# Performance work log

Measured on AMD Instinct MI355X. Metric: run time of the kernel, lower is better.

The kernel has to match this reference:

```python
import jax, jax.numpy as jnp
import numpy as np

N = 100000   # nodes
E = 1600000  # edges (avg degree 16)
DIM = 3      # coordinate dims
R = 3        # pseudo-coordinate dim
C = 32       # channels / Gaussian kernels
F = 64       # non-coordinate node features


def setup_inputs() -> dict:
    key = jax.random.key(0)
    k1, k2, k3, k4, k5 = jax.random.split(key, 5)
    features = jax.random.normal(k1, (N, DIM + F), dtype=jnp.float32)
    edge_index = jax.random.randint(k2, (E, 2), 0, N, dtype=jnp.int32)  # (row=i, col=j) per edge
    w_dense = jax.random.normal(k3, (DIM, R), dtype=jnp.float32) / jnp.sqrt(jnp.float32(DIM))  # lecun-ish
    b_dense = jnp.zeros((R,), dtype=jnp.float32)
    mu = jax.random.normal(k4, (C, N, R), dtype=jnp.float32) * 0.1
    # sigma initialized positive (abs of lecun normal in the original); keep bounded away from 0
    sig = jax.random.uniform(k5, (C, N, R), dtype=jnp.float32, minval=0.1, maxval=1.0)
    return {"features": features, "edge_index": edge_index,
            "w_dense": w_dense, "b_dense": b_dense, "mu": mu, "sig": sig}


def reference(features, edge_index, w_dense, b_dense, mu, sig):
    coords = features[:, :DIM]          # [N, 3]
    h = features[:, DIM:]               # [N, F]
    src = edge_index[:, 0]              # row index i per edge
    dst = edge_index[:, 1]              # col index j per edge
    # per-edge pseudo-coordinates: tanh(Dense_r(x_j - x_i))
    u = jnp.tanh((coords[dst] - coords[src]) @ w_dense + b_dense)      # [E, R]
    # Gaussian-mixture edge weight per (channel, edge), mu/sigma gathered at row node i
    diff = u[None, :, :] - mu[:, src, :]                               # [C, E, R]
    w = jnp.exp(-0.5 * jnp.sum(diff * diff / sig[:, src, :], axis=-1)) # [C, E]
    # (A o W) @ H summed over feature axis == sum_j w[c,i,j] * sum_f H[j,f]
    msg = w * jnp.sum(h, axis=-1)[dst][None, :]                        # [C, E]
    agg = jax.ops.segment_sum(msg.T, src, num_segments=N)              # [N, C]
    return jnp.concatenate([coords, agg], axis=-1)                     # [N, DIM + C]
```

## Files before the change

kernel.cpp:

```cpp
#include <hip/hip_runtime.h>

#define DIMV 3
#define RV 3
#define CV 32
#define FV 64
#define ROWF 67
#define ROWO 35
#define CAP 64
#define SCAN_T 1024

__device__ __forceinline__ float fast_tanh(float x) {
    float ex = __expf(2.0f * x);
    return (ex - 1.0f) * __builtin_amdgcn_rcpf(ex + 1.0f);
}

__global__ void prep_kernel(const float* __restrict__ features,
                            float4* __restrict__ nd,
                            int* __restrict__ counts,
                            float* __restrict__ out, int N) {
    int gid = blockIdx.x * blockDim.x + threadIdx.x;
    if (gid < N) counts[gid] = 0;
    int node = gid >> 6;
    int lane = threadIdx.x & 63;
    if (node >= N) return;
    const float* row = features + (size_t)node * ROWF;
    float f0 = row[lane];
    float f1 = (lane < ROWF - 64) ? row[64 + lane] : 0.0f;
    float v = (lane >= DIMV ? f0 : 0.0f) + f1;
    for (int off = 32; off > 0; off >>= 1) v += __shfl_xor(v, off, 64);
    float c0 = __shfl(f0, 0, 64);
    float c1 = __shfl(f0, 1, 64);
    float c2 = __shfl(f0, 2, 64);
    if (lane == 0) nd[node] = make_float4(c0, c1, c2, v);
    if (lane < DIMV) out[(size_t)node * ROWO + lane] = f0;
}

__global__ void scatter_pad_kernel(const int2* __restrict__ ei2,
                                   const float4* __restrict__ nd,
                                   const float* __restrict__ wd,
                                   const float* __restrict__ bd,
                                   int* __restrict__ counts,
                                   float4* __restrict__ ue_pad, int E) {
    int e = blockIdx.x * blockDim.x + threadIdx.x;
    if (e >= E) return;
    int2 sd = ei2[e];
    int k = atomicAdd(counts + sd.x, 1);
    if (k >= CAP) k = CAP - 1;
    float4 ps = nd[sd.x];
    float4 pd = nd[sd.y];
    float dx = pd.x - ps.x, dy = pd.y - ps.y, dz = pd.z - ps.z;
    float u0 = fast_tanh(dx * wd[0] + dy * wd[3] + dz * wd[6] + bd[0]);
    float u1 = fast_tanh(dx * wd[1] + dy * wd[4] + dz * wd[7] + bd[1]);
    float u2 = fast_tanh(dx * wd[2] + dy * wd[5] + dz * wd[8] + bd[2]);
    ue_pad[(size_t)sd.x * CAP + k] = make_float4(u0, u1, u2, pd.w);
}

__global__ void node_pad_kernel(const int* __restrict__ counts,
                                const float4* __restrict__ ue_pad,
                                const float* __restrict__ mu,
                                const float* __restrict__ sig,
                                float* __restrict__ out, int N) {
    __shared__ float4 sm[4][CAP];
    int node = (blockIdx.x * blockDim.x + threadIdx.x) >> 6;
    int lane = threadIdx.x & 63;
    int w = threadIdx.x >> 6;
    int c = lane & 31;
    int half = lane >> 5;
    bool valid = node < N;
    float m0 = 0, m1 = 0, m2 = 0, i0 = 1, i1 = 1, i2 = 1;
    int cnt = 0;
    if (valid) {
        size_t slab = (size_t)N * RV;
        const float* mp = mu + (size_t)c * slab + (size_t)node * RV;
        const float* sp = sig + (size_t)c * slab + (size_t)node * RV;
        m0 = mp[0]; m1 = mp[1]; m2 = mp[2];
        i0 = __builtin_amdgcn_rcpf(sp[0]);
        i1 = __builtin_amdgcn_rcpf(sp[1]);
        i2 = __builtin_amdgcn_rcpf(sp[2]);
        cnt = counts[node];
        if (cnt > CAP) cnt = CAP;
        if (lane < cnt) sm[w][lane] = ue_pad[(size_t)node * CAP + lane];
    }
    __syncthreads();
    float acc = 0.0f;
    for (int k = half; k < cnt; k += 2) {
        float4 q = sm[w][k];
        float d0 = q.x - m0, d1 = q.y - m1, d2 = q.z - m2;
        float t = d0 * d0 * i0 + d1 * d1 * i1 + d2 * d2 * i2;
        acc += __expf(-0.5f * t) * q.w;
    }
    acc += __shfl_xor(acc, 32, 64);
    if (valid && half == 0) out[(size_t)node * ROWO + DIMV + c] = acc;
}


__global__ void hist_kernel(const int2* __restrict__ ei2, int* __restrict__ counts, int E) {
    int e = blockIdx.x * blockDim.x + threadIdx.x;
    if (e >= E) return;
    atomicAdd(counts + ei2[e].x, 1);
}

__global__ void scan_a_kernel(const int* __restrict__ counts, int* __restrict__ offsets,
                              int* __restrict__ partials, int N) {
    __shared__ int sm[SCAN_T];
    int t = threadIdx.x;
    int i = blockIdx.x * SCAN_T + t;
    int c = (i < N) ? counts[i] : 0;
    sm[t] = c;
    __syncthreads();
    for (int off = 1; off < SCAN_T; off <<= 1) {
        int v = (t >= off) ? sm[t - off] : 0;
        __syncthreads();
        sm[t] += v;
        __syncthreads();
    }
    if (i < N) offsets[i] = sm[t] - c;
    if (t == SCAN_T - 1) partials[blockIdx.x] = sm[t];
}

__global__ void scan_b_kernel(int* __restrict__ partials, int B) {
    __shared__ int sm[SCAN_T];
    int t = threadIdx.x;
    int c = (t < B) ? partials[t] : 0;
    sm[t] = c;
    __syncthreads();
    for (int off = 1; off < SCAN_T; off <<= 1) {
        int v = (t >= off) ? sm[t - off] : 0;
        __syncthreads();
        sm[t] += v;
        __syncthreads();
    }
    if (t < B) partials[t] = sm[t] - c;
}

__global__ void scan_c_kernel(int* __restrict__ offsets, const int* __restrict__ partials,
                              int* __restrict__ cursor, int N, int E) {
    int i = blockIdx.x * blockDim.x + threadIdx.x;
    if (i == 0) offsets[N] = E;
    if (i >= N) return;
    int off = offsets[i] + partials[i / SCAN_T];
    offsets[i] = off;
    cursor[i] = off;
}

__global__ void scatter_u_kernel(const int2* __restrict__ ei2, int* __restrict__ cursor,
                                 const float4* __restrict__ nd,
                                 const float* __restrict__ wd, const float* __restrict__ bd,
                                 float4* __restrict__ ue, int E) {
    int e = blockIdx.x * blockDim.x + threadIdx.x;
    if (e >= E) return;
    int2 sd = ei2[e];
    int pos = atomicAdd(cursor + sd.x, 1);
    float4 ps = nd[sd.x];
    float4 pd = nd[sd.y];
    float dx = pd.x - ps.x, dy = pd.y - ps.y, dz = pd.z - ps.z;
    float u0 = fast_tanh(dx * wd[0] + dy * wd[3] + dz * wd[6] + bd[0]);
    float u1 = fast_tanh(dx * wd[1] + dy * wd[4] + dz * wd[7] + bd[1]);
    float u2 = fast_tanh(dx * wd[2] + dy * wd[5] + dz * wd[8] + bd[2]);
    ue[pos] = make_float4(u0, u1, u2, pd.w);
}

__global__ void node_acc2_kernel(const int* __restrict__ offsets,
                                 const float4* __restrict__ ue,
                                 const float* __restrict__ mu,
                                 const float* __restrict__ sig,
                                 float* __restrict__ out, int N) {
    int node = (blockIdx.x * blockDim.x + threadIdx.x) >> 6;
    if (node >= N) return;
    int lane = threadIdx.x & 63;
    int c = lane & 31;
    int half = lane >> 5;
    size_t slab = (size_t)N * RV;
    const float* mp = mu + (size_t)c * slab + (size_t)node * RV;
    const float* sp = sig + (size_t)c * slab + (size_t)node * RV;
    float m0 = mp[0], m1 = mp[1], m2 = mp[2];
    float i0 = __builtin_amdgcn_rcpf(sp[0]);
    float i1 = __builtin_amdgcn_rcpf(sp[1]);
    float i2 = __builtin_amdgcn_rcpf(sp[2]);
    int off0 = offsets[node], off1 = offsets[node + 1];
    float acc = 0.0f;
    for (int i = off0 + half; i < off1; i += 2) {
        float4 q = ue[i];
        float d0 = q.x - m0, d1 = q.y - m1, d2 = q.z - m2;
        float t = d0 * d0 * i0 + d1 * d1 * i1 + d2 * d2 * i2;
        acc += __expf(-0.5f * t) * q.w;
    }
    acc += __shfl_xor(acc, 32, 64);
    if (half == 0) out[(size_t)node * ROWO + DIMV + c] = acc;
}


__global__ void fb_pre_kernel(const float* __restrict__ features,
                              float4* __restrict__ nd, float* __restrict__ out, int N) {
    int gid = blockIdx.x * blockDim.x + threadIdx.x;
    int node = gid >> 6;
    int lane = threadIdx.x & 63;
    if (node >= N) return;
    const float* row = features + (size_t)node * ROWF;
    float f0 = row[lane];
    float f1 = (lane < ROWF - 64) ? row[64 + lane] : 0.0f;
    float v = (lane >= DIMV ? f0 : 0.0f) + f1;
    for (int off = 32; off > 0; off >>= 1) v += __shfl_xor(v, off, 64);
    float c0 = __shfl(f0, 0, 64);
    float c1 = __shfl(f0, 1, 64);
    float c2 = __shfl(f0, 2, 64);
    if (lane == 0) nd[node] = make_float4(c0, c1, c2, v);
    float* orow = out + (size_t)node * ROWO;
    if (lane < DIMV) orow[lane] = f0;
    else if (lane < ROWO) orow[lane] = 0.0f;
}

__global__ void fb_edge_kernel(const int* __restrict__ ei, const float4* __restrict__ nd,
                               const float* __restrict__ wd, const float* __restrict__ bd,
                               const float* __restrict__ mu, const float* __restrict__ sig,
                               float* __restrict__ out, int N, int E) {
    int e = blockIdx.x * blockDim.x + threadIdx.x;
    if (e >= E) return;
    int s = ei[2 * e];
    int d = ei[2 * e + 1];
    float4 ps = nd[s];
    float4 pd = nd[d];
    float dx = pd.x - ps.x, dy = pd.y - ps.y, dz = pd.z - ps.z;
    float u0 = fast_tanh(dx * wd[0] + dy * wd[3] + dz * wd[6] + bd[0]);
    float u1 = fast_tanh(dx * wd[1] + dy * wd[4] + dz * wd[7] + bd[1]);
    float u2 = fast_tanh(dx * wd[2] + dy * wd[5] + dz * wd[8] + bd[2]);
    float hs = pd.w;
    float* oagg = out + (size_t)s * ROWO + DIMV;
    size_t nodeoff = (size_t)s * RV;
    size_t slab = (size_t)N * RV;
#pragma unroll 4
    for (int c = 0; c < CV; ++c) {
        const float* mp = mu + (size_t)c * slab + nodeoff;
        const float* sp = sig + (size_t)c * slab + nodeoff;
        float d0 = u0 - mp[0], d1 = u1 - mp[1], d2 = u2 - mp[2];
        float t = d0 * d0 * __builtin_amdgcn_rcpf(sp[0])
                + d1 * d1 * __builtin_amdgcn_rcpf(sp[1])
                + d2 * d2 * __builtin_amdgcn_rcpf(sp[2]);
        atomicAdd(oagg + c, __expf(-0.5f * t) * hs);
    }
}

extern "C" void kernel_launch(void* const* d_in, const int* in_sizes, int n_in,
                              void* d_out, int out_size, void* d_ws, size_t ws_size,
                              hipStream_t stream) {
    const float* features = (const float*)d_in[0];
    const int*   ei       = (const int*)d_in[1];
    const int2*  ei2      = (const int2*)d_in[1];
    const float* wd       = (const float*)d_in[2];
    const float* bd       = (const float*)d_in[3];
    const float* mu       = (const float*)d_in[4];
    const float* sig      = (const float*)d_in[5];
    float* out = (float*)d_out;

    int N = in_sizes[0] / ROWF;
    int E = in_sizes[1] / 2;
    int B = (N + SCAN_T - 1) / SCAN_T;

    size_t cur = 0;
    auto take = [&](size_t bytes) { size_t p = cur; cur += (bytes + 255) & ~(size_t)255; return p; };
    size_t o_nd      = take((size_t)N * sizeof(float4));
    size_t o_counts  = take((size_t)N * sizeof(int));
    size_t o_offsets = take((size_t)(N + 1) * sizeof(int));
    size_t o_cursor  = take((size_t)N * sizeof(int));
    size_t o_part    = take((size_t)SCAN_T * sizeof(int));
    size_t o_tail    = cur;
    size_t need_pad  = o_tail + (((size_t)N * CAP * sizeof(float4) + 255) & ~(size_t)255);
    size_t need_full = o_tail + (((size_t)E * sizeof(float4) + 255) & ~(size_t)255);

    char* ws = (char*)d_ws;
    float4* nd   = (float4*)(ws + o_nd);
    int* counts  = (int*)(ws + o_counts);
    int* offsets = (int*)(ws + o_offsets);
    int* cursor  = (int*)(ws + o_cursor);
    int* part    = (int*)(ws + o_part);

    if (ws_size >= need_pad) {
        float4* ue_pad = (float4*)(ws + o_tail);
        prep_kernel<<<(N + 3) / 4, 256, 0, stream>>>(features, nd, counts, out, N);
        scatter_pad_kernel<<<(E + 255) / 256, 256, 0, stream>>>(ei2, nd, wd, bd, counts, ue_pad, E);
        node_pad_kernel<<<(N + 3) / 4, 256, 0, stream>>>(counts, ue_pad, mu, sig, out, N);
    } else if (ws_size >= need_full && B <= SCAN_T) {
        float4* ue = (float4*)(ws + o_tail);
        prep_kernel<<<(N + 3) / 4, 256, 0, stream>>>(features, nd, counts, out, N);
        hist_kernel<<<(E + 255) / 256, 256, 0, stream>>>(ei2, counts, E);
        scan_a_kernel<<<B, SCAN_T, 0, stream>>>(counts, offsets, part, N);
        scan_b_kernel<<<1, SCAN_T, 0, stream>>>(part, B);
        scan_c_kernel<<<(N + 255) / 256, 256, 0, stream>>>(offsets, part, cursor, N, E);
        scatter_u_kernel<<<(E + 255) / 256, 256, 0, stream>>>(ei2, cursor, nd, wd, bd, ue, E);
        node_acc2_kernel<<<(N + 3) / 4, 256, 0, stream>>>(offsets, ue, mu, sig, out, N);
    } else {
        fb_pre_kernel<<<(N + 3) / 4, 256, 0, stream>>>(features, nd, out, N);
        fb_edge_kernel<<<(E + 255) / 256, 256, 0, stream>>>(ei, nd, wd, bd, mu, sig, out, N, E);
    }
}
```

Measured before the change: 277.4 us.

## Scatter only destination indices into padded buckets; compute pseudo-coords in node kernel

The scatter pass now writes a 4-byte destination index per edge into the padded per-node buckets instead of a 16-byte float4 of tanh pseudo-coordinates and feature sums. It also reads edge pairs with a nontemporal load. The node kernel gathers the node and neighbour float4 records itself and computes the tanh projection before staging results in shared memory. This shrinks the padded workspace and the scatter write traffic, but moves random neighbour gathers into the node kernel and has every lane load a slot even when it is unused (clamped to a valid node).

```diff
diff --git a/kernel.cpp b/kernel.cpp
--- a/kernel.cpp
+++ b/kernel.cpp
@@ -36,27 +36,24 @@
 }
 
 __global__ void scatter_pad_kernel(const int2* __restrict__ ei2,
-                                   const float4* __restrict__ nd,
-                                   const float* __restrict__ wd,
-                                   const float* __restrict__ bd,
                                    int* __restrict__ counts,
-                                   float4* __restrict__ ue_pad, int E) {
+                                   int* __restrict__ dst_pad, int E) {
     int e = blockIdx.x * blockDim.x + threadIdx.x;
     if (e >= E) return;
-    int2 sd = ei2[e];
-    int k = atomicAdd(counts + sd.x, 1);
+    unsigned long long v =
+        __builtin_nontemporal_load((const unsigned long long*)ei2 + e);
+    int s = (int)(v & 0xffffffffull);
+    int d = (int)(v >> 32);
+    int k = atomicAdd(counts + s, 1);
     if (k >= CAP) k = CAP - 1;
-    float4 ps = nd[sd.x];
-    float4 pd = nd[sd.y];
-    float dx = pd.x - ps.x, dy = pd.y - ps.y, dz = pd.z - ps.z;
-    float u0 = fast_tanh(dx * wd[0] + dy * wd[3] + dz * wd[6] + bd[0]);
-    float u1 = fast_tanh(dx * wd[1] + dy * wd[4] + dz * wd[7] + bd[1]);
-    float u2 = fast_tanh(dx * wd[2] + dy * wd[5] + dz * wd[8] + bd[2]);
-    ue_pad[(size_t)sd.x * CAP + k] = make_float4(u0, u1, u2, pd.w);
+    dst_pad[(size_t)s * CAP + k] = d;
 }
 
 __global__ void node_pad_kernel(const int* __restrict__ counts,
-                                const float4* __restrict__ ue_pad,
+                                const int* __restrict__ dst_pad,
+                                const float4* __restrict__ nd,
+                                const float* __restrict__ wd,
+                                const float* __restrict__ bd,
                                 const float* __restrict__ mu,
                                 const float* __restrict__ sig,
                                 float* __restrict__ out, int N) {
@@ -77,9 +74,19 @@
         i0 = __builtin_amdgcn_rcpf(sp[0]);
         i1 = __builtin_amdgcn_rcpf(sp[1]);
         i2 = __builtin_amdgcn_rcpf(sp[2]);
+        int d = dst_pad[(size_t)node * CAP + lane];
         cnt = counts[node];
         if (cnt > CAP) cnt = CAP;
-        if (lane < cnt) sm[w][lane] = ue_pad[(size_t)node * CAP + lane];
+        d = (d < 0) ? 0 : (d >= N ? N - 1 : d);
+        float4 pn = nd[node];
+        float4 pd = nd[d];
+        if (lane < cnt) {
+            float dx = pd.x - pn.x, dy = pd.y - pn.y, dz = pd.z - pn.z;
+            float u0 = fast_tanh(dx * wd[0] + dy * wd[3] + dz * wd[6] + bd[0]);
+            float u1 = fast_tanh(dx * wd[1] + dy * wd[4] + dz * wd[7] + bd[1]);
+            float u2 = fast_tanh(dx * wd[2] + dy * wd[5] + dz * wd[8] + bd[2]);
+            sm[w][lane] = make_float4(u0, u1, u2, pd.w);
+        }
     }
     __syncthreads();
     float acc = 0.0f;
@@ -264,7 +271,7 @@
     size_t o_cursor  = take((size_t)N * sizeof(int));
     size_t o_part    = take((size_t)SCAN_T * sizeof(int));
     size_t o_tail    = cur;
-    size_t need_pad  = o_tail + (((size_t)N * CAP * sizeof(float4) + 255) & ~(size_t)255);
+    size_t need_pad  = o_tail + (((size_t)N * CAP * sizeof(int) + 255) & ~(size_t)255);
     size_t need_full = o_tail + (((size_t)E * sizeof(float4) + 255) & ~(size_t)255);
 
     char* ws = (char*)d_ws;
@@ -275,10 +282,10 @@
     int* part    = (int*)(ws + o_part);
 
     if (ws_size >= need_pad) {
-        float4* ue_pad = (float4*)(ws + o_tail);
+        int* dst_pad = (int*)(ws + o_tail);
         prep_kernel<<<(N + 3) / 4, 256, 0, stream>>>(features, nd, counts, out, N);
-        scatter_pad_kernel<<<(E + 255) / 256, 256, 0, stream>>>(ei2, nd, wd, bd, counts, ue_pad, E);
-        node_pad_kernel<<<(N + 3) / 4, 256, 0, stream>>>(counts, ue_pad, mu, sig, out, N);
+        scatter_pad_kernel<<<(E + 255) / 256, 256, 0, stream>>>(ei2, counts, dst_pad, E);
+        node_pad_kernel<<<(N + 3) / 4, 256, 0, stream>>>(counts, dst_pad, nd, wd, bd, mu, sig, out, N);
     } else if (ws_size >= need_full && B <= SCAN_T) {
         float4* ue = (float4*)(ws + o_tail);
         prep_kernel<<<(N + 3) / 4, 256, 0, stream>>>(features, nd, counts, out, N);
```

After: 324.2 us. +16.9%, slower.
